# Kernel optimization log

Hardware: AMD Instinct MI355X
Metric: run time of the kernel (lower is better)

The kernel has to match this reference:

```python
import jax, jax.numpy as jnp
import numpy as np

N_NODES = 100000
N_EDGES = 1600000
N_GRAPHS = 128
D = 128          # input_dim == hidden_dim
OUT = 64         # output_dim (num classes)
L = 4            # num_layers - 1 GIN message-passing layers
BN_EPS = 1e-5


def setup_inputs() -> dict:
    key = jax.random.key(0)
    ks = jax.random.split(key, 12)
    s = 1.0 / np.sqrt(D)
    x = jax.random.normal(ks[0], (N_NODES, D), jnp.float32)
    edge_src = jax.random.randint(ks[1], (N_GRAPHS * 0 + N_EDGES,), 0, N_NODES, jnp.int32)
    edge_dst = jax.random.randint(ks[2], (N_EDGES,), 0, N_NODES, jnp.int32)
    graph_ids = jnp.sort(jax.random.randint(ks[3], (N_NODES,), 0, N_GRAPHS, jnp.int32))
    return {
        'x': x,
        'edge_src': edge_src,
        'edge_dst': edge_dst,
        'graph_ids': graph_ids,
        'eps': jnp.zeros((L,), jnp.float32),
        'W1': jax.random.normal(ks[4], (L, D, D), jnp.float32) * s,
        'b1': jnp.zeros((L, D), jnp.float32),
        'g1': jnp.ones((L, D), jnp.float32),
        'be1': jnp.zeros((L, D), jnp.float32),
        'W2': jax.random.normal(ks[5], (L, D, D), jnp.float32) * s,
        'b2': jnp.zeros((L, D), jnp.float32),
        'g2': jnp.ones((L, D), jnp.float32),
        'be2': jnp.zeros((L, D), jnp.float32),
        'predW': jax.random.normal(ks[6], (L + 1, D, OUT), jnp.float32) * s,
        'predb': jnp.zeros((L + 1, OUT), jnp.float32),
    }


def _bn(h, g, b):
    # BatchNorm1d in training mode: batch mean / biased variance over nodes
    mu = jnp.mean(h, axis=0)
    var = jnp.var(h, axis=0)
    return g * (h - mu) * jax.lax.rsqrt(var + BN_EPS) + b


def reference(x, edge_src, edge_dst, graph_ids, eps, W1, b1, g1, be1,
              W2, b2, g2, be2, predW, predb):
    n = x.shape[0]
    hidden = [x]
    h = x
    for l in range(L):
        # sparse Adj @ h : gather neighbor feats at edges, scatter-add to dst
        agg = jax.ops.segment_sum(h[edge_src], edge_dst, num_segments=n)
        pooled = agg + (1.0 + eps[l]) * h                      # GIN eps update
        z = jax.nn.relu(_bn(pooled @ W1[l] + b1[l], g1[l], be1[l]))  # MLP hidden
        z = z @ W2[l] + b2[l]                                  # MLP out
        h = jax.nn.relu(_bn(z, g2[l], be2[l]))                 # outer BN + relu
        hidden.append(h)
    # GIN readout: sum graph pooling + per-layer linear prediction (dropout p=0)
    score = jnp.zeros((N_GRAPHS, OUT), jnp.float32)
    for l, hl in enumerate(hidden):
        pooled_g = jax.ops.segment_sum(hl, graph_ids, num_segments=N_GRAPHS)
        score = score + pooled_g @ predW[l] + predb[l]
    return score
```

## Files before the change

### kernel.cpp

```cpp
#include <hip/hip_runtime.h>

#define NN 100000
#define NE 1600000
#define NG 128
#define DIM 128
#define OUTD 64
#define NL 4
#define SLCAP 48
#define RPB 256
#define RPBLKS ((NN + RPB - 1) / RPB)

typedef __attribute__((ext_vector_type(8))) short bf16x8;
typedef __attribute__((ext_vector_type(4))) float floatx4;

__device__ __forceinline__ float bf_lo(unsigned u) {
    union { unsigned u; float f; } c; c.u = u << 16; return c.f;
}
__device__ __forceinline__ float bf_hi(unsigned u) {
    union { unsigned u; float f; } c; c.u = u & 0xffff0000u; return c.f;
}
__device__ __forceinline__ unsigned f2bf(float x) {
    union { float f; unsigned u; } c; c.f = x;
    return (c.u + 0x7fffu + ((c.u >> 16) & 1u)) >> 16;
}
__device__ __forceinline__ float bfs2f(short s) {
    union { unsigned u; float f; } c; c.u = ((unsigned)(unsigned short)s) << 16; return c.f;
}

__device__ __forceinline__ void bn_coef(const float* __restrict__ stat,
                                        const float* __restrict__ gamma,
                                        const float* __restrict__ beta,
                                        int f, float& a, float& c) {
    float mu = stat[f] * (1.0f / NN);
    float var = fmaf(-mu, mu, stat[DIM + f] * (1.0f / NN));
    a = gamma[f] * rsqrtf(var + 1e-5f);
    c = fmaf(-mu, a, beta[f]);
}

__global__ void build_links(const int* __restrict__ esrc, const int* __restrict__ edst,
                            int* __restrict__ head, int2* __restrict__ link) {
    int e = blockIdx.x * 256 + threadIdx.x;
    if (e < NE) {
        int d = edst[e];
        int prev = atomicExch(&head[d], e);
        link[e] = make_int2(prev, esrc[e]);
    }
}

__global__ __launch_bounds__(256)
void repack_slots(const int* __restrict__ head, const int2* __restrict__ link,
                  int* __restrict__ cnt, int* __restrict__ slot) {
    __shared__ int ls[SLCAP][RPB + 1];
    const int tid = threadIdx.x;
    const int n = blockIdx.x * RPB + tid;
    if (n < NN) {
        int e = head[n];
        int c = 0;
        while (e >= 0 && c < SLCAP) {
            int2 pr = link[e];
            ls[c][tid] = pr.y;
            e = pr.x;
            ++c;
        }
        cnt[n] = c;
    }
    __syncthreads();
    const int base = blockIdx.x * (RPB * SLCAP);
    for (int i = tid; i < RPB * SLCAP; i += 256) {
        int row = i / SLCAP, col = i - row * SLCAP;
        slot[base + i] = ls[col][row];
    }
}

__global__ void to_bf16(const float* __restrict__ x, unsigned* __restrict__ xb) {
    size_t i = ((size_t)blockIdx.x * 256 + threadIdx.x) * 4;
    float4 v = *(const float4*)(x + i);
    uint2 o;
    o.x = f2bf(v.x) | (f2bf(v.y) << 16);
    o.y = f2bf(v.z) | (f2bf(v.w) << 16);
    *(uint2*)(xb + i / 2) = o;
}

__global__ void build_wt(const float* __restrict__ W1, const float* __restrict__ W2,
                         unsigned short* __restrict__ Wt) {
    int b = blockIdx.x;
    const float* W = ((b & 1) ? W2 : W1) + (size_t)(b >> 1) * DIM * DIM;
    unsigned short* O = Wt + (size_t)b * DIM * DIM;
    int i = blockIdx.y * 2048 + threadIdx.x;
    for (int j = 0; j < 8; ++j, i += 256) {
        int k = i >> 7, n = i & 127;
        O[n * DIM + k] = (unsigned short)f2bf(W[i]);
    }
}

__global__ void csr_agg(const unsigned* __restrict__ hq, const int* __restrict__ cnt,
                        const int* __restrict__ slot, const float* __restrict__ eps, int l,
                        unsigned* __restrict__ outq) {
    const int t = threadIdx.x;
    const int node = blockIdx.x * 4 + (t >> 6);
    const int lane = t & 63;
    const int chunk = lane & 15;
    const int grp = lane >> 4;
    const uint4* __restrict__ h4 = (const uint4*)hq;

    const int deg = cnt[node];

    float acc[8];
    {
        uint4 sv = h4[(size_t)node * 16 + chunk];
        float e1 = (grp == 0) ? (1.0f + eps[l]) : 0.0f;
        const unsigned* p = (const unsigned*)&sv;
#pragma unroll
        for (int q = 0; q < 4; ++q) {
            acc[2 * q]     = e1 * bf_lo(p[q]);
            acc[2 * q + 1] = e1 * bf_hi(p[q]);
        }
    }

    if (deg > 0) {
        const int iters = (deg + 15) >> 4;
        const int base = node * SLCAP;
        const int hi = base + deg - 1;
        const int j0 = base + grp;
        int idx[4];
#pragma unroll
        for (int q = 0; q < 4; ++q) {
            int j = j0 + q * 4;
            int v = slot[min(j, hi)];
            idx[q] = (j <= hi) ? v : NN;
        }

        for (int it = 0; it < iters; ++it) {
            uint4 u[4];
#pragma unroll
            for (int q = 0; q < 4; ++q) u[q] = h4[(size_t)idx[q] * 16 + chunk];

            if (it + 1 < iters) {
                const int jn = j0 + (it + 1) * 16;
#pragma unroll
                for (int q = 0; q < 4; ++q) {
                    int j = jn + q * 4;
                    int v = slot[min(j, hi)];
                    idx[q] = (j <= hi) ? v : NN;
                }
            }

#pragma unroll
            for (int q = 0; q < 4; ++q) {
                const unsigned* p = (const unsigned*)&u[q];
#pragma unroll
                for (int r = 0; r < 4; ++r) {
                    acc[2 * r]     += bf_lo(p[r]);
                    acc[2 * r + 1] += bf_hi(p[r]);
                }
            }
        }
    }

#pragma unroll
    for (int r = 0; r < 8; ++r) {
        acc[r] += __shfl_xor(acc[r], 16);
        acc[r] += __shfl_xor(acc[r], 32);
    }
    if (grp == 0) {
        uint4 o;
        unsigned* po = (unsigned*)&o;
#pragma unroll
        for (int r = 0; r < 4; ++r)
            po[r] = f2bf(acc[2 * r]) | (f2bf(acc[2 * r + 1]) << 16);
        ((uint4*)outq)[(size_t)node * 16 + chunk] = o;
    }
}

template<int TR>
__global__ __launch_bounds__(256, 2)
void gemm_mfma(const unsigned short* __restrict__ X, const unsigned short* __restrict__ Wt,
               const float* __restrict__ bias,
               const float* __restrict__ stat, const float* __restrict__ gamma,
               const float* __restrict__ beta,
               unsigned short* __restrict__ Y, float* __restrict__ ostat) {
    __shared__ unsigned short Ws[DIM * DIM];
    __shared__ float tatc[2 * DIM];
    float* red = (float*)Ws;
    const int t = threadIdx.x;
    const int w = t >> 6, lane = t & 63;
    const int quad = lane >> 4, m = lane & 15;
    const int rowbase = blockIdx.x * 128 + w * 32;

#pragma unroll
    for (int i = 0; i < 8; ++i) {
        int chunk = t + i * 256;
        int r = chunk >> 4, c = chunk & 15;
        ((uint4*)Ws)[(r << 4) | (c ^ (r & 15))] = ((const uint4*)Wt)[chunk];
    }
    if (TR && t < DIM) {
        float a, c;
        bn_coef(stat, gamma, beta, t, a, c);
        tatc[t] = a; tatc[DIM + t] = c;
    }

    bf16x8 a[2][4];
#pragma unroll
    for (int rt = 0; rt < 2; ++rt) {
        int row = rowbase + rt * 16 + m;
        if (row > NN - 1) row = NN - 1;
        const unsigned short* xr = X + (size_t)row * DIM + quad * 8;
#pragma unroll
        for (int ks = 0; ks < 4; ++ks)
            a[rt][ks] = *(const bf16x8*)(xr + ks * 32);
    }
    __syncthreads();
    if (TR) {
#pragma unroll
        for (int rt = 0; rt < 2; ++rt)
#pragma unroll
            for (int ks = 0; ks < 4; ++ks) {
                int kk = ks * 32 + quad * 8;
                bf16x8 v = a[rt][ks];
#pragma unroll
                for (int j = 0; j < 8; ++j) {
                    float fv = bfs2f(v[j]);
                    fv = fmaxf(fmaf(fv, tatc[kk + j], tatc[DIM + kk + j]), 0.f);
                    v[j] = (short)f2bf(fv);
                }
                a[rt][ks] = v;
            }
    }

    floatx4 acc[2][8];
#pragma unroll
    for (int rt = 0; rt < 2; ++rt)
#pragma unroll
        for (int ct = 0; ct < 8; ++ct) acc[rt][ct] = (floatx4)0.f;

#pragma unroll
    for (int ct = 0; ct < 8; ++ct) {
        const int row = ct * 16 + m;
        const bf16x8* wrow = (const bf16x8*)&Ws[row * DIM];
#pragma unroll
        for (int ks = 0; ks < 4; ++ks) {
            bf16x8 b = wrow[(ks * 4 + quad) ^ m];
            acc[0][ct] = __builtin_amdgcn_mfma_f32_16x16x32_bf16(a[0][ks], b, acc[0][ct], 0, 0, 0);
            acc[1][ct] = __builtin_amdgcn_mfma_f32_16x16x32_bf16(a[1][ks], b, acc[1][ct], 0, 0, 0);
        }
    }

    float sv[8], qv[8];
#pragma unroll
    for (int ct = 0; ct < 8; ++ct) {
        int col = ct * 16 + m;
        float bv = bias[col];
        float s = 0.f, q = 0.f;
#pragma unroll
        for (int rt = 0; rt < 2; ++rt) {
#pragma unroll
            for (int r = 0; r < 4; ++r) {
                int row = rowbase + rt * 16 + quad * 4 + r;
                float val = acc[rt][ct][r] + bv;
                if (row < NN) {
                    Y[(size_t)row * DIM + col] = (unsigned short)f2bf(val);
                    s += val;
                    q = fmaf(val, val, q);
                }
            }
        }
        s += __shfl_xor(s, 16); s += __shfl_xor(s, 32);
        q += __shfl_xor(q, 16); q += __shfl_xor(q, 32);
        sv[ct] = s; qv[ct] = q;
    }
    __syncthreads();
#pragma unroll
    for (int ct = 0; ct < 8; ++ct) {
        int col = ct * 16 + m;
        if (quad == 0) { red[w * 256 + col] = sv[ct]; red[w * 256 + 128 + col] = qv[ct]; }
    }
    __syncthreads();
    if (t < 256) {
        float tot = red[t] + red[256 + t] + red[512 + t] + red[768 + t];
        unsafeAtomicAdd(&ostat[t], tot);
    }
}

template<int TR>
__global__ void pool_nodes(const unsigned* __restrict__ hq, const int* __restrict__ gid,
                           const float* __restrict__ stat, const float* __restrict__ gamma,
                           const float* __restrict__ beta, float* __restrict__ pg) {
    const int lane = threadIdx.x;
    int start = blockIdx.x * 32;
    int end = start + 32;
    if (end > NN) end = NN;
    int f = lane * 2;
    float a0 = 0.f, c0 = 0.f, a1 = 0.f, c1 = 0.f;
    if (TR) {
        bn_coef(stat, gamma, beta, f, a0, c0);
        bn_coef(stat, gamma, beta, f + 1, a1, c1);
    }
    int cur = gid[start];
    float acc0 = 0.f, acc1 = 0.f;
    for (int i = start; i < end; ++i) {
        int g = gid[i];
        if (g != cur) {
            unsafeAtomicAdd(&pg[cur * DIM + f], acc0);
            unsafeAtomicAdd(&pg[cur * DIM + f + 1], acc1);
            acc0 = 0.f; acc1 = 0.f;
            cur = g;
        }
        unsigned u = hq[(size_t)i * 64 + lane];
        float x0 = bf_lo(u), x1 = bf_hi(u);
        if (TR) {
            x0 = fmaxf(fmaf(x0, a0, c0), 0.f);
            x1 = fmaxf(fmaf(x1, a1, c1), 0.f);
        }
        acc0 += x0; acc1 += x1;
    }
    unsafeAtomicAdd(&pg[cur * DIM + f], acc0);
    unsafeAtomicAdd(&pg[cur * DIM + f + 1], acc1);
}

template<int WRITE>
__global__ void norm_pool(const unsigned* __restrict__ hq, const int* __restrict__ gid,
                          const float* __restrict__ stat, const float* __restrict__ gamma,
                          const float* __restrict__ beta,
                          unsigned* __restrict__ outq, float* __restrict__ pg) {
    const int lane = threadIdx.x;
    int start = blockIdx.x * 32;
    int end = start + 32;
    if (end > NN) end = NN;
    int f = lane * 2;
    float a0, c0, a1, c1;
    bn_coef(stat, gamma, beta, f, a0, c0);
    bn_coef(stat, gamma, beta, f + 1, a1, c1);
    int cur = gid[start];
    float acc0 = 0.f, acc1 = 0.f;
    for (int i = start; i < end; ++i) {
        int g = gid[i];
        if (g != cur) {
            unsafeAtomicAdd(&pg[cur * DIM + f], acc0);
            unsafeAtomicAdd(&pg[cur * DIM + f + 1], acc1);
            acc0 = 0.f; acc1 = 0.f;
            cur = g;
        }
        unsigned u = hq[(size_t)i * 64 + lane];
        float x0 = fmaxf(fmaf(bf_lo(u), a0, c0), 0.f);
        float x1 = fmaxf(fmaf(bf_hi(u), a1, c1), 0.f);
        if (WRITE)
            outq[(size_t)i * 64 + lane] = f2bf(x0) | (f2bf(x1) << 16);
        acc0 += x0; acc1 += x1;
    }
    unsafeAtomicAdd(&pg[cur * DIM + f], acc0);
    unsafeAtomicAdd(&pg[cur * DIM + f + 1], acc1);
}

__global__ void final_score(const float* __restrict__ pg, const float* __restrict__ predW,
                            const float* __restrict__ predb, float* __restrict__ out) {
    int g = blockIdx.x;
    int o = threadIdx.x;
    float acc = 0.f;
    for (int l = 0; l <= NL; ++l) {
        acc += predb[l * OUTD + o];
        const float* pgr = pg + ((size_t)l * NG + g) * DIM;
        const float* w = predW + (size_t)l * DIM * OUTD;
#pragma unroll 8
        for (int k = 0; k < DIM; ++k)
            acc = fmaf(pgr[k], w[k * OUTD + o], acc);
    }
    out[g * OUTD + o] = acc;
}

extern "C" void kernel_launch(void* const* d_in, const int* in_sizes, int n_in,
                              void* d_out, int out_size, void* d_ws, size_t ws_size,
                              hipStream_t stream) {
    const float* x     = (const float*)d_in[0];
    const int*   esrc  = (const int*)d_in[1];
    const int*   edst  = (const int*)d_in[2];
    const int*   gid   = (const int*)d_in[3];
    const float* eps   = (const float*)d_in[4];
    const float* W1    = (const float*)d_in[5];
    const float* b1    = (const float*)d_in[6];
    const float* g1    = (const float*)d_in[7];
    const float* be1   = (const float*)d_in[8];
    const float* W2    = (const float*)d_in[9];
    const float* b2    = (const float*)d_in[10];
    const float* g2    = (const float*)d_in[11];
    const float* be2   = (const float*)d_in[12];
    const float* predW = (const float*)d_in[13];
    const float* predb = (const float*)d_in[14];
    float* out = (float*)d_out;

    unsigned short* XB = (unsigned short*)d_ws;
    unsigned short* A  = XB + (size_t)(NN + 1) * DIM;
    unsigned short* B  = A + (size_t)NN * DIM;
    unsigned short* WT = B + (size_t)NN * DIM;
    float* PG    = (float*)(WT + 8 * DIM * DIM);
    float* STATS = PG + 5 * NG * DIM;
    int* CNT  = (int*)(STATS + NL * 512);
    int* SLOT = CNT + NN;
    int*  HEAD = (int*)B;
    int2* LINK = (int2*)(HEAD + NN);

    hipMemsetAsync(PG, 0, (5 * NG * DIM + NL * 512) * sizeof(float), stream);
    hipMemsetAsync(XB + (size_t)NN * DIM, 0, DIM * sizeof(unsigned short), stream);
    hipMemsetAsync(HEAD, 0xFF, NN * sizeof(int), stream);

    build_links<<<(NE + 255) / 256, 256, 0, stream>>>(esrc, edst, HEAD, LINK);
    repack_slots<<<RPBLKS, 256, 0, stream>>>(HEAD, LINK, CNT, SLOT);
    to_bf16<<<(NN * DIM) / 1024, 256, 0, stream>>>(x, (unsigned*)XB);
    build_wt<<<dim3(8, 8), 256, 0, stream>>>(W1, W2, WT);

    const int poolBlocks = (NN + 31) / 32;
    const int aggBlocks  = (NN + 3) / 4;
    const int gemmBlocks = (NN + 127) / 128;

    for (int l = 0; l < NL; ++l) {
        float* STATL = STATS + l * 512;
        if (l == 0) {
            pool_nodes<0><<<poolBlocks, 64, 0, stream>>>((const unsigned*)XB, gid,
                                                         nullptr, nullptr, nullptr, PG);
        } else {
            const float* prevS = STATS + (l - 1) * 512 + 256;
            norm_pool<1><<<poolBlocks, 64, 0, stream>>>((const unsigned*)A, gid, prevS,
                                                        g2 + (l - 1) * DIM, be2 + (l - 1) * DIM,
                                                        (unsigned*)XB, PG + l * NG * DIM);
        }
        csr_agg<<<aggBlocks, 256, 0, stream>>>((const unsigned*)XB, CNT, SLOT, eps, l,
                                               (unsigned*)B);
        gemm_mfma<0><<<gemmBlocks, 256, 0, stream>>>(B, WT + (size_t)(2 * l) * DIM * DIM,
                                                     b1 + l * DIM, nullptr, nullptr, nullptr,
                                                     B, STATL);
        gemm_mfma<1><<<gemmBlocks, 256, 0, stream>>>(B, WT + (size_t)(2 * l + 1) * DIM * DIM,
                                                     b2 + l * DIM, STATL, g1 + l * DIM,
                                                     be1 + l * DIM, A, STATL + 256);
    }
    norm_pool<0><<<poolBlocks, 64, 0, stream>>>((const unsigned*)A, gid,
                                                STATS + (NL - 1) * 512 + 256,
                                                g2 + (NL - 1) * DIM, be2 + (NL - 1) * DIM,
                                                nullptr, PG + NL * NG * DIM);
    final_score<<<NG, OUTD, 0, stream>>>(PG, predW, predb, out);
}
```

Baseline: 848.5 us.

## Store node features in feature-panel layout so aggregation gathers fit cache

Splits the node feature matrices into 8 panels of 16 bf16 features (about 3.2 MB each). Each aggregation kernel launch now handles one panel per blockIdx.x, with 16 edges in flight per wave and 8-byte gathers, so a panel's randomly gathered rows can stay resident in L2/MALL. The GEMM, pooling and conversion kernels are changed to read and write the panel layout. The cost is 8x more aggregation blocks, redundant slot-index reads for each panel, and narrower, less coalesced GEMM loads and stores.

```diff
diff --git a/kernel.cpp b/kernel.cpp
--- a/kernel.cpp
+++ b/kernel.cpp
@@ -9,6 +9,8 @@
 #define SLCAP 48
 #define RPB 256
 #define RPBLKS ((NN + RPB - 1) / RPB)
+#define PSTRD ((NN + 1) * 8)
+#define PSTRS ((NN + 1) * 16)
 
 typedef __attribute__((ext_vector_type(8))) short bf16x8;
 typedef __attribute__((ext_vector_type(4))) float floatx4;
@@ -73,12 +75,18 @@
 }
 
 __global__ void to_bf16(const float* __restrict__ x, unsigned* __restrict__ xb) {
-    size_t i = ((size_t)blockIdx.x * 256 + threadIdx.x) * 4;
-    float4 v = *(const float4*)(x + i);
+    int idx = blockIdx.x * 256 + threadIdx.x;
+    int n = idx >> 5, g = idx & 31;
+    float4 v = *(const float4*)(x + (size_t)idx * 4);
     uint2 o;
     o.x = f2bf(v.x) | (f2bf(v.y) << 16);
     o.y = f2bf(v.z) | (f2bf(v.w) << 16);
-    *(uint2*)(xb + i / 2) = o;
+    *(uint2*)(xb + (size_t)(g >> 2) * PSTRD + n * 8 + 2 * (g & 3)) = o;
+}
+
+__global__ void zero_rows(unsigned* __restrict__ xb) {
+    int t = threadIdx.x;
+    xb[(size_t)(t >> 3) * PSTRD + (size_t)NN * 8 + (t & 7)] = 0;
 }
 
 __global__ void build_wt(const float* __restrict__ W1, const float* __restrict__ W2,
@@ -97,78 +105,49 @@
                         const int* __restrict__ slot, const float* __restrict__ eps, int l,
                         unsigned* __restrict__ outq) {
     const int t = threadIdx.x;
-    const int node = blockIdx.x * 4 + (t >> 6);
+    const int node = blockIdx.y * 4 + (t >> 6);
     const int lane = t & 63;
-    const int chunk = lane & 15;
-    const int grp = lane >> 4;
-    const uint4* __restrict__ h4 = (const uint4*)hq;
+    const int sub = lane & 3;
+    const int eg = lane >> 2;
+    const unsigned pb = blockIdx.x * (unsigned)PSTRD;
+    const uint2* __restrict__ h2 = (const uint2*)(hq + pb);
 
     const int deg = cnt[node];
-
-    float acc[8];
+    float a0, a1, a2, a3;
     {
-        uint4 sv = h4[(size_t)node * 16 + chunk];
-        float e1 = (grp == 0) ? (1.0f + eps[l]) : 0.0f;
-        const unsigned* p = (const unsigned*)&sv;
-#pragma unroll
-        for (int q = 0; q < 4; ++q) {
-            acc[2 * q]     = e1 * bf_lo(p[q]);
-            acc[2 * q + 1] = e1 * bf_hi(p[q]);
-        }
+        uint2 sv = h2[node * 4 + sub];
+        float e1 = (eg == 0) ? (1.0f + eps[l]) : 0.0f;
+        a0 = e1 * bf_lo(sv.x); a1 = e1 * bf_hi(sv.x);
+        a2 = e1 * bf_lo(sv.y); a3 = e1 * bf_hi(sv.y);
     }
 
     if (deg > 0) {
         const int iters = (deg + 15) >> 4;
         const int base = node * SLCAP;
         const int hi = base + deg - 1;
-        const int j0 = base + grp;
-        int idx[4];
-#pragma unroll
-        for (int q = 0; q < 4; ++q) {
-            int j = j0 + q * 4;
-            int v = slot[min(j, hi)];
-            idx[q] = (j <= hi) ? v : NN;
-        }
-
+        int j = base + eg;
+        int idx = (j <= hi) ? slot[min(j, hi)] : NN;
         for (int it = 0; it < iters; ++it) {
-            uint4 u[4];
-#pragma unroll
-            for (int q = 0; q < 4; ++q) u[q] = h4[(size_t)idx[q] * 16 + chunk];
-
+            uint2 u = h2[idx * 4 + sub];
             if (it + 1 < iters) {
-                const int jn = j0 + (it + 1) * 16;
-#pragma unroll
-                for (int q = 0; q < 4; ++q) {
-                    int j = jn + q * 4;
-                    int v = slot[min(j, hi)];
-                    idx[q] = (j <= hi) ? v : NN;
-                }
+                int jn = base + (it + 1) * 16 + eg;
+                idx = (jn <= hi) ? slot[min(jn, hi)] : NN;
             }
-
-#pragma unroll
-            for (int q = 0; q < 4; ++q) {
-                const unsigned* p = (const unsigned*)&u[q];
-#pragma unroll
-                for (int r = 0; r < 4; ++r) {
-                    acc[2 * r]     += bf_lo(p[r]);
-                    acc[2 * r + 1] += bf_hi(p[r]);
-                }
-            }
-        }
-    }
-
-#pragma unroll
-    for (int r = 0; r < 8; ++r) {
-        acc[r] += __shfl_xor(acc[r], 16);
-        acc[r] += __shfl_xor(acc[r], 32);
-    }
-    if (grp == 0) {
-        uint4 o;
-        unsigned* po = (unsigned*)&o;
-#pragma unroll
-        for (int r = 0; r < 4; ++r)
-            po[r] = f2bf(acc[2 * r]) | (f2bf(acc[2 * r + 1]) << 16);
-        ((uint4*)outq)[(size_t)node * 16 + chunk] = o;
+            a0 += bf_lo(u.x); a1 += bf_hi(u.x);
+            a2 += bf_lo(u.y); a3 += bf_hi(u.y);
+        }
+    }
+
+#pragma unroll
+    for (int s = 4; s < 64; s <<= 1) {
+        a0 += __shfl_xor(a0, s); a1 += __shfl_xor(a1, s);
+        a2 += __shfl_xor(a2, s); a3 += __shfl_xor(a3, s);
+    }
+    if (eg == 0) {
+        uint2 o;
+        o.x = f2bf(a0) | (f2bf(a1) << 16);
+        o.y = f2bf(a2) | (f2bf(a3) << 16);
+        ((uint2*)(outq + pb))[node * 4 + sub] = o;
     }
 }
 
@@ -204,10 +183,12 @@
     for (int rt = 0; rt < 2; ++rt) {
         int row = rowbase + rt * 16 + m;
         if (row > NN - 1) row = NN - 1;
-        const unsigned short* xr = X + (size_t)row * DIM + quad * 8;
-#pragma unroll
-        for (int ks = 0; ks < 4; ++ks)
-            a[rt][ks] = *(const bf16x8*)(xr + ks * 32);
+#pragma unroll
+        for (int ks = 0; ks < 4; ++ks) {
+            const unsigned short* p = X + (size_t)(2 * ks + (quad >> 1)) * PSTRS
+                                        + (size_t)row * 16 + (quad & 1) * 8;
+            a[rt][ks] = *(const bf16x8*)p;
+        }
     }
     __syncthreads();
     if (TR) {
@@ -258,7 +239,7 @@
                 int row = rowbase + rt * 16 + quad * 4 + r;
                 float val = acc[rt][ct][r] + bv;
                 if (row < NN) {
-                    Y[(size_t)row * DIM + col] = (unsigned short)f2bf(val);
+                    Y[(size_t)ct * PSTRS + (size_t)row * 16 + m] = (unsigned short)f2bf(val);
                     s += val;
                     q = fmaf(val, val, q);
                 }
@@ -290,6 +271,7 @@
     int end = start + 32;
     if (end > NN) end = NN;
     int f = lane * 2;
+    const size_t abase = (size_t)(lane >> 3) * PSTRD + (lane & 7);
     float a0 = 0.f, c0 = 0.f, a1 = 0.f, c1 = 0.f;
     if (TR) {
         bn_coef(stat, gamma, beta, f, a0, c0);
@@ -305,7 +287,7 @@
             acc0 = 0.f; acc1 = 0.f;
             cur = g;
         }
-        unsigned u = hq[(size_t)i * 64 + lane];
+        unsigned u = hq[abase + (size_t)i * 8];
         float x0 = bf_lo(u), x1 = bf_hi(u);
         if (TR) {
             x0 = fmaxf(fmaf(x0, a0, c0), 0.f);
@@ -327,6 +309,7 @@
     int end = start + 32;
     if (end > NN) end = NN;
     int f = lane * 2;
+    const size_t abase = (size_t)(lane >> 3) * PSTRD + (lane & 7);
     float a0, c0, a1, c1;
     bn_coef(stat, gamma, beta, f, a0, c0);
     bn_coef(stat, gamma, beta, f + 1, a1, c1);
@@ -340,11 +323,11 @@
             acc0 = 0.f; acc1 = 0.f;
             cur = g;
         }
-        unsigned u = hq[(size_t)i * 64 + lane];
+        unsigned u = hq[abase + (size_t)i * 8];
         float x0 = fmaxf(fmaf(bf_lo(u), a0, c0), 0.f);
         float x1 = fmaxf(fmaf(bf_hi(u), a1, c1), 0.f);
         if (WRITE)
-            outq[(size_t)i * 64 + lane] = f2bf(x0) | (f2bf(x1) << 16);
+            outq[abase + (size_t)i * 8] = f2bf(x0) | (f2bf(x1) << 16);
         acc0 += x0; acc1 += x1;
     }
     unsafeAtomicAdd(&pg[cur * DIM + f], acc0);
@@ -389,8 +372,8 @@
 
     unsigned short* XB = (unsigned short*)d_ws;
     unsigned short* A  = XB + (size_t)(NN + 1) * DIM;
-    unsigned short* B  = A + (size_t)NN * DIM;
-    unsigned short* WT = B + (size_t)NN * DIM;
+    unsigned short* B  = A + (size_t)(NN + 1) * DIM;
+    unsigned short* WT = B + (size_t)(NN + 1) * DIM;
     float* PG    = (float*)(WT + 8 * DIM * DIM);
     float* STATS = PG + 5 * NG * DIM;
     int* CNT  = (int*)(STATS + NL * 512);
@@ -399,17 +382,17 @@
     int2* LINK = (int2*)(HEAD + NN);
 
     hipMemsetAsync(PG, 0, (5 * NG * DIM + NL * 512) * sizeof(float), stream);
-    hipMemsetAsync(XB + (size_t)NN * DIM, 0, DIM * sizeof(unsigned short), stream);
     hipMemsetAsync(HEAD, 0xFF, NN * sizeof(int), stream);
 
     build_links<<<(NE + 255) / 256, 256, 0, stream>>>(esrc, edst, HEAD, LINK);
     repack_slots<<<RPBLKS, 256, 0, stream>>>(HEAD, LINK, CNT, SLOT);
-    to_bf16<<<(NN * DIM) / 1024, 256, 0, stream>>>(x, (unsigned*)XB);
+    to_bf16<<<(NN * 32) / 256, 256, 0, stream>>>(x, (unsigned*)XB);
+    zero_rows<<<1, 64, 0, stream>>>((unsigned*)XB);
     build_wt<<<dim3(8, 8), 256, 0, stream>>>(W1, W2, WT);
 
     const int poolBlocks = (NN + 31) / 32;
-    const int aggBlocks  = (NN + 3) / 4;
     const int gemmBlocks = (NN + 127) / 128;
+    const dim3 aggGrid(8, NN / 4);
 
     for (int l = 0; l < NL; ++l) {
         float* STATL = STATS + l * 512;
@@ -422,8 +405,8 @@
                                                         g2 + (l - 1) * DIM, be2 + (l - 1) * DIM,
                                                         (unsigned*)XB, PG + l * NG * DIM);
         }
-        csr_agg<<<aggBlocks, 256, 0, stream>>>((const unsigned*)XB, CNT, SLOT, eps, l,
-                                               (unsigned*)B);
+        csr_agg<<<aggGrid, 256, 0, stream>>>((const unsigned*)XB, CNT, SLOT, eps, l,
+                                             (unsigned*)B);
         gemm_mfma<0><<<gemmBlocks, 256, 0, stream>>>(B, WT + (size_t)(2 * l) * DIM * DIM,
                                                      b1 + l * DIM, nullptr, nullptr, nullptr,
                                                      B, STATL);
```

Result: slower. 1.356 ms (+59.8%).
